# Kernel tuning notes

Measured on AMD Instinct MI355X. Metric: run time of the kernel, lower is better.

## Reference

```python
import jax, jax.numpy as jnp
import numpy as np
import math

N_NODES, N_EDGES, NNZ, D, L = 100000, 20000, 500000, 128, 4
ALPHA, LAMDA = 0.1, 0.5


def setup_inputs() -> dict:
    key = jax.random.key(0)
    ks = jax.random.split(key, 16)
    x = jax.random.normal(ks[0], (N_NODES, D), jnp.float32)
    e = jax.random.normal(ks[1], (N_EDGES, D), jnp.float32)
    nodes = jax.random.randint(ks[2], (NNZ,), 0, N_NODES)
    edges = jnp.sort(jax.random.randint(ks[3], (NNZ,), 0, N_EDGES)).at[-1].set(N_EDGES - 1)
    hyperedge_index = jnp.stack([nodes, edges]).astype(jnp.int32)
    dist_v2e = jax.random.randint(ks[4], (NNZ,), 0, 64).astype(jnp.float32)
    deg_v2e = jax.random.randint(ks[5], (NNZ,), 0, 64).astype(jnp.float32)
    dist_e2v = jax.random.randint(ks[6], (NNZ,), 0, 64).astype(jnp.float32)
    deg_e2v = jax.random.randint(ks[7], (NNZ,), 0, 64).astype(jnp.float32)
    s = 0.05
    W0 = jax.random.normal(ks[8], (D, D), jnp.float32) * s
    b0 = jnp.zeros((D,), jnp.float32)
    Wn = jax.random.normal(ks[9], (L, D, D), jnp.float32) * s
    We = jax.random.normal(ks[10], (L, D, D), jnp.float32) * s
    attn_w = jax.random.normal(ks[11], (L, 2 * D), jnp.float32) * s
    attn_b = jnp.zeros((L,), jnp.float32)
    wd_w = jax.random.normal(ks[12], (L,), jnp.float32) * s
    wd_b = jnp.zeros((L,), jnp.float32)
    wg_w = jax.random.normal(ks[13], (L,), jnp.float32) * s
    wg_b = jnp.zeros((L,), jnp.float32)
    return dict(x=x, e=e, hyperedge_index=hyperedge_index, dist_v2e=dist_v2e,
                deg_v2e=deg_v2e, dist_e2v=dist_e2v, deg_e2v=deg_e2v,
                W0=W0, b0=b0, Wn=Wn, We=We, attn_w=attn_w, attn_b=attn_b,
                wd_w=wd_w, wd_b=wd_b, wg_w=wg_w, wg_b=wg_b)


def _seg_softmax(s, idx, num):
    # numerically-stable scatter_softmax over segments idx
    m = jax.ops.segment_max(s, idx, num_segments=num)
    ex = jnp.exp(s - m[idx])
    den = jax.ops.segment_sum(ex, idx, num_segments=num)
    return ex / den[idx]


def _forward(x, e, hei, dv2e, gv2e, de2v, ge2v, W0, b0, Wn, We, aw, ab, wdw, wdb, wgw, wgb):
    nodes, edges = hei[0], hei[1]
    N, E = x.shape[0], e.shape[0]
    ones = jnp.ones(nodes.shape[0], x.dtype)
    dV = jax.ops.segment_sum(ones, nodes, num_segments=N)
    cnt = jax.ops.segment_sum(ones, edges, num_segments=E)
    dE = jax.ops.segment_sum(dV[nodes], edges, num_segments=E) / jnp.maximum(cnt, 1.0)
    degV = jnp.where(dV > 0, dV ** -0.5, 1.0)[:, None]   # [N,1]
    degE = jnp.where(dE > 0, dE ** -0.5, 1.0)[:, None]   # [E,1]

    x = jax.nn.relu(x @ W0 + b0)
    x0, e0 = x, e
    d = x.shape[1]
    for i in range(L):
        beta = math.log(LAMDA / (i + 1) + 1.0)
        # v2e attention: concat [x[nodes], e[edges]] -> softmax over edge segments
        sx1 = x @ aw[i, :d]; se1 = e @ aw[i, d:]
        s_v2e = sx1[nodes] + se1[edges] + ab[i] + dv2e * wdw[i] + wdb[i] + gv2e * wgw[i] + wgb[i]
        a_v2e = _seg_softmax(s_v2e, edges, E)[:, None]
        # e2v attention (flipped): concat [e[edges], x[nodes]] -> softmax over node segments
        se2 = e @ aw[i, :d]; sx2 = x @ aw[i, d:]
        s_e2v = se2[edges] + sx2[nodes] + ab[i] + de2v * wdw[i] + wdb[i] + ge2v * wgw[i] + wgb[i]
        a_e2v = _seg_softmax(s_e2v, nodes, N)[:, None]

        Xe1 = jax.ops.segment_sum(x[nodes] * a_v2e, edges, num_segments=E) * degE
        Xv1 = jax.ops.segment_sum(Xe1[edges] * a_e2v, nodes, num_segments=N) * degV
        Xv2 = jax.ops.segment_sum(e[edges] * a_e2v, nodes, num_segments=N) * degV
        Xe2 = jax.ops.segment_sum(Xv2[nodes] * a_v2e, edges, num_segments=E) * degE
        xm = (Xv1 + Xv2) * 0.5
        em = (Xe1 + Xe2) * 0.5
        xi = (1 - ALPHA) * xm + ALPHA * x0
        x = (1 - beta) * xi + beta * (xi @ Wn[i])
        ei = (1 - ALPHA) * em + ALPHA * e0
        e = (1 - beta) * ei + beta * (ei @ We[i])
        if i < L - 1:
            x = jax.nn.relu(x)
            e = jax.nn.relu(e)
    return x, e


def reference(x, e, hyperedge_index, dist_v2e, deg_v2e, dist_e2v, deg_e2v,
              W0, b0, Wn, We, attn_w, attn_b, wd_w, wd_b, wg_w, wg_b):
    return _forward(x, e, hyperedge_index, dist_v2e, deg_v2e, dist_e2v, deg_e2v,
                    W0, b0, Wn, We, attn_w, attn_b, wd_w, wd_b, wg_w, wg_b)
```

## Files before the change

### kernel.cpp

```cpp
#include <hip/hip_runtime.h>
#include <hip/hip_fp16.h>
#include <math.h>

#define DD 128
#define SCAN_BLOCKS 256
#define SMAX_CAP 128

typedef _Float16 f16x8 __attribute__((ext_vector_type(8)));
typedef float f32x4 __attribute__((ext_vector_type(4)));

__device__ inline float wave_sum(float v){
#pragma unroll
  for (int m = 32; m >= 1; m >>= 1) v += __shfl_xor(v, m, 64);
  return v;
}
__device__ inline int wave_sum_i(int v){
#pragma unroll
  for (int m = 32; m >= 1; m >>= 1) v += __shfl_xor(v, m, 64);
  return v;
}


__global__ void k_edge_offsets(const int* __restrict__ edges, int nnz, int E,
                               int* __restrict__ eo){
  int e = blockIdx.x * blockDim.x + threadIdx.x;
  if (e > E) return;
  int lo = 0, hi = nnz;
  while (lo < hi){ int mid = (lo + hi) >> 1; if (edges[mid] < e) lo = mid + 1; else hi = mid; }
  eo[e] = lo;
}

__global__ void k_hist(const int* __restrict__ nodes, int nnz, int* __restrict__ dV){
  int k = blockIdx.x * blockDim.x + threadIdx.x;
  if (k < nnz) atomicAdd(&dV[nodes[k]], 1);
}

__global__ __launch_bounds__(256) void k_scan_partial(const int* __restrict__ dV, int N,
                                                      int* __restrict__ part){
  int b = blockIdx.x, t = threadIdx.x;
  int chunk = (N + SCAN_BLOCKS - 1) / SCAN_BLOCKS;
  int s0 = b * chunk, s1 = min(s0 + chunk, N);
  int sum = 0;
  for (int n = s0 + t; n < s1; n += 256) sum += dV[n];
  sum = wave_sum_i(sum);
  __shared__ int wred[4];
  int lane = t & 63, wid = t >> 6;
  if (lane == 0) wred[wid] = sum;
  __syncthreads();
  if (t == 0) part[b] = wred[0] + wred[1] + wred[2] + wred[3];
}

__global__ __launch_bounds__(SCAN_BLOCKS) void k_scan_blocksums(int* __restrict__ part){
  __shared__ int sh[SCAN_BLOCKS];
  int t = threadIdx.x;
  int v = part[t];
  sh[t] = v; __syncthreads();
  for (int off = 1; off < SCAN_BLOCKS; off <<= 1){
    int add = (t >= off) ? sh[t - off] : 0;
    __syncthreads();
    sh[t] += add;
    __syncthreads();
  }
  part[t] = sh[t] - v;
}

__global__ __launch_bounds__(256) void k_scan_apply(const int* __restrict__ dV, int N, int nnz,
    const int* __restrict__ partScan, int* __restrict__ no, int* __restrict__ nfill,
    float* __restrict__ degV){
  int b = blockIdx.x, t = threadIdx.x;
  int chunk = (N + SCAN_BLOCKS - 1) / SCAN_BLOCKS;
  int s0 = b * chunk, s1 = min(s0 + chunk, N);
  int lane = t & 63, wid = t >> 6;
  __shared__ int wtot[4];
  __shared__ int s_run;
  if (t == 0) s_run = partScan[b];
  __syncthreads();
  for (int base = s0; base < s1; base += 256){
    int n = base + t;
    int d = (n < s1) ? dV[n] : 0;
    int v = d;
#pragma unroll
    for (int off = 1; off < 64; off <<= 1){
      int o = __shfl_up(v, off, 64);
      if (lane >= off) v += o;
    }
    if (lane == 63) wtot[wid] = v;
    __syncthreads();
    int run0 = s_run;
    int woff = 0;
    for (int w = 0; w < wid; w++) woff += wtot[w];
    if (n < s1){
      int excl = run0 + woff + v - d;
      no[n] = excl; nfill[n] = excl;
      degV[n] = d > 0 ? 1.0f / sqrtf((float)d) : 1.0f;
    }
    int btot = wtot[0] + wtot[1] + wtot[2] + wtot[3];
    __syncthreads();
    if (t == 0) s_run = run0 + btot;
    __syncthreads();
  }
  if (b == 0 && t == 0) no[N] = nnz;
}

__global__ void k_permpack(const int* __restrict__ nodes, const int* __restrict__ edges,
                           const float* __restrict__ dist, const float* __restrict__ deg,
                           int nnz, int* __restrict__ nfill, float2* __restrict__ pack){
  int k = blockIdx.x * blockDim.x + threadIdx.x;
  if (k < nnz){
    int pos = atomicAdd(&nfill[nodes[k]], 1);
    pack[pos] = make_float2(__int_as_float(edges[k]), dist[k] + 64.f * deg[k]);
  }
}

__global__ void k_edge_deg(const int* __restrict__ nodes, const int* __restrict__ eo, int E,
                           const int* __restrict__ dV, float* __restrict__ degE){
  int e = blockIdx.x * blockDim.x + threadIdx.x;
  if (e >= E) return;
  int b = eo[e], en = eo[e + 1];
  float s = 0.f;
  for (int k = b; k < en; k++) s += (float)dV[nodes[k]];
  float cnt = (float)(en - b);
  float dE = s / fmaxf(cnt, 1.0f);
  degE[e] = dE > 0.f ? 1.0f / sqrtf(dE) : 1.0f;
}

__global__ __launch_bounds__(256) void k_einit(const float2* __restrict__ e_in2,
    const float* __restrict__ aw1, const float* __restrict__ aw2,
    int E, __half2* __restrict__ ET, __half2* __restrict__ e0h,
    float* __restrict__ se1, float* __restrict__ se2){
  int wave = threadIdx.x >> 6, lane = threadIdx.x & 63;
  int e = blockIdx.x * 4 + wave;
  if (e >= E) return;
  float2 v = e_in2[(size_t)e * 64 + lane];
  __half2 h = __floats2half2_rn(v.x, v.y);
  ET[(size_t)e * 128 + 2 * lane + 1] = h;
  e0h[(size_t)e * 64 + lane] = h;
  float2 a2v = ((const float2*)aw2)[lane];
  float2 a1v = ((const float2*)aw1)[lane];
  float s1 = v.x * a2v.x + v.y * a2v.y;
  float s2 = v.x * a1v.x + v.y * a1v.y;
  s1 = wave_sum(s1); s2 = wave_sum(s2);
  if (lane == 0){ se1[e] = s1; se2[e] = s2; }
}

__global__ void k_wcast(const float* __restrict__ W0, const float* __restrict__ Wn,
                        const float* __restrict__ We, _Float16* __restrict__ Wt){
  int idx = blockIdx.x * 256 + threadIdx.x;
  if (idx >= 9 * 16384) return;
  int m = idx >> 14, r = idx & 16383;
  int n = r >> 7, k = r & 127;
  float v;
  if (m == 0){
    v = W0[k * 128 + n];
  } else {
    int i = (m <= 4) ? m - 1 : m - 5;
    const float* src = (m <= 4) ? Wn + (size_t)i * 16384 : We + (size_t)i * 16384;
    float beta = logf(0.5f / (float)(i + 1) + 1.0f);
    v = beta * src[k * 128 + n] + ((n == k) ? (1.0f - beta) : 0.f);
  }
  Wt[(size_t)m * 16384 + n * 128 + k] = (_Float16)v;
}


__device__ inline void acc8h(const float4 q, float w, float* a){
  float2 h0 = __half22float2(*(const __half2*)&q.x);
  float2 h1 = __half22float2(*(const __half2*)&q.y);
  float2 h2v = __half22float2(*(const __half2*)&q.z);
  float2 h3 = __half22float2(*(const __half2*)&q.w);
  a[0] += w * h0.x; a[1] += w * h0.y; a[2] += w * h1.x; a[3] += w * h1.y;
  a[4] += w * h2v.x; a[5] += w * h2v.y; a[6] += w * h3.x; a[7] += w * h3.y;
}

__global__ __launch_bounds__(256) void k_sma1(
    const int* __restrict__ nodes, const int* __restrict__ eo,
    const float* __restrict__ sx1, const float* __restrict__ se1,
    const float* __restrict__ dist, const float* __restrict__ deg,
    const float* __restrict__ ab, const float* __restrict__ wdw, const float* __restrict__ wdb,
    const float* __restrict__ wgw, const float* __restrict__ wgb, int li,
    const float* __restrict__ degE, const float4* __restrict__ xh4,
    int E, float* __restrict__ a_v2e, float* __restrict__ esc, __half2* __restrict__ ET){
  __shared__ float lw[8][SMAX_CAP];
  int l32 = threadIdx.x & 31;
  int grp = threadIdx.x >> 5;
  int e = blockIdx.x * 8 + grp;
  if (e >= E) return;
  int b = eo[e], en = eo[e + 1];
  int l16 = l32 & 15, hf = l32 >> 4;
  if (b >= en){
    if (l32 == 0) esc[e] = 0.f;
    if (hf == 0){
      __half2 z = __floats2half2_rn(0.f, 0.f);
      size_t o = (size_t)e * 128 + 8 * l16;
      ET[o] = z; ET[o + 2] = z; ET[o + 4] = z; ET[o + 6] = z;
    }
    return;
  }
  float base = se1[e] + ab[li] + wdb[li] + wgb[li];
  float wd = wdw[li], wg = wgw[li];
  float m = -INFINITY;
  float sreg[4];
#pragma unroll
  for (int c = 0; c < 4; c++){
    int k = b + l32 + 32 * c;
    if (k < en){
      float s = sx1[nodes[k]] + base + dist[k] * wd + deg[k] * wg;
      sreg[c] = s; m = fmaxf(m, s);
    }
  }
  for (int k = b + l32 + SMAX_CAP; k < en; k += 32){
    float s = sx1[nodes[k]] + base + dist[k] * wd + deg[k] * wg;
    m = fmaxf(m, s);
  }
#pragma unroll
  for (int mm = 16; mm >= 1; mm >>= 1) m = fmaxf(m, __shfl_xor(m, mm, 32));
  float sum = 0.f;
#pragma unroll
  for (int c = 0; c < 4; c++){
    int k = b + l32 + 32 * c;
    if (k < en){
      float ex = __expf(sreg[c] - m);
      a_v2e[k] = ex; lw[grp][l32 + 32 * c] = ex; sum += ex;
    }
  }
  for (int k = b + l32 + SMAX_CAP; k < en; k += 32){
    float s = sx1[nodes[k]] + base + dist[k] * wd + deg[k] * wg;
    float ex = __expf(s - m);
    a_v2e[k] = ex; sum += ex;
  }
#pragma unroll
  for (int mm = 16; mm >= 1; mm >>= 1) sum += __shfl_xor(sum, mm, 32);
  float sc = degE[e] / sum;
  if (l32 == 0) esc[e] = sc;
  float a[8] = {0.f, 0.f, 0.f, 0.f, 0.f, 0.f, 0.f, 0.f};
  int k = b + hf;
  for (; k + 2 < en; k += 4){
    int n0 = nodes[k], n1 = nodes[k + 2];
    float w0 = (k - b < SMAX_CAP) ? lw[grp][k - b] : a_v2e[k];
    float w1 = (k + 2 - b < SMAX_CAP) ? lw[grp][k + 2 - b] : a_v2e[k + 2];
    float4 v0 = xh4[(size_t)n0 * 16 + l16];
    float4 v1 = xh4[(size_t)n1 * 16 + l16];
    acc8h(v0, w0, a); acc8h(v1, w1, a);
  }
  for (; k < en; k += 2){
    int n = nodes[k];
    float w = (k - b < SMAX_CAP) ? lw[grp][k - b] : a_v2e[k];
    float4 v = xh4[(size_t)n * 16 + l16];
    acc8h(v, w, a);
  }
#pragma unroll
  for (int j = 0; j < 8; j++) a[j] += __shfl_xor(a[j], 16, 32);
  if (hf == 0){
    size_t o = (size_t)e * 128 + 8 * l16;
    ET[o]     = __floats2half2_rn(a[0] * sc, a[1] * sc);
    ET[o + 2] = __floats2half2_rn(a[2] * sc, a[3] * sc);
    ET[o + 4] = __floats2half2_rn(a[4] * sc, a[5] * sc);
    ET[o + 6] = __floats2half2_rn(a[6] * sc, a[7] * sc);
  }
}

__device__ inline void acc8(const float4 q, float w, float* a1, float* a2){
  float2 x0 = __half22float2(*(const __half2*)&q.x);
  float2 e0 = __half22float2(*(const __half2*)&q.y);
  float2 x1 = __half22float2(*(const __half2*)&q.z);
  float2 e1 = __half22float2(*(const __half2*)&q.w);
  a1[0] += w * x0.x; a1[1] += w * x0.y; a1[2] += w * x1.x; a1[3] += w * x1.y;
  a2[0] += w * e0.x; a2[1] += w * e0.y; a2[2] += w * e1.x; a2[3] += w * e1.y;
}

__global__ __launch_bounds__(256) void k_agg2f(
    const float2* __restrict__ pack, const int* __restrict__ no,
    const float* __restrict__ se2, const float* __restrict__ sx2,
    const float* __restrict__ ab, const float* __restrict__ wdw, const float* __restrict__ wdb,
    const float* __restrict__ wgw, const float* __restrict__ wgb, int li,
    const float4* __restrict__ ETq,
    const float* __restrict__ degV, const __half2* __restrict__ x0h,
    int N, __half2* __restrict__ Xv2h, __half2* __restrict__ xiH){
  int l32 = threadIdx.x & 31;
  int grp = threadIdx.x >> 5;
  int n = blockIdx.x * 8 + grp;
  if (n >= N) return;
  int b = no[n], en = no[n + 1];
  float base = sx2[n] + ab[li] + wdb[li] + wgb[li];
  float wd = wdw[li], wg = wgw[li];
  float2 x0v2 = *(const float2*)&x0h[(size_t)n * 64 + 2 * l32];
  float l_run = 0.f;
  float a1[4] = {0.f, 0.f, 0.f, 0.f}, a2[4] = {0.f, 0.f, 0.f, 0.f};
  if (en - b <= 32){
    int cs = en - b;
    float s = -INFINITY; int e_l = 0;
    if (l32 < cs){
      float2 pk = pack[b + l32];
      e_l = __float_as_int(pk.x);
      int vi = (int)pk.y;
      s = se2[e_l] + base + (float)(vi & 63) * wd + (float)(vi >> 6) * wg;
    }
    float m_c = s;
#pragma unroll
    for (int mm = 16; mm >= 1; mm >>= 1) m_c = fmaxf(m_c, __shfl_xor(m_c, mm, 32));
    float p = (l32 < cs) ? __expf(s - m_c) : 0.f;
    l_run = p;
#pragma unroll
    for (int mm = 16; mm >= 1; mm >>= 1) l_run += __shfl_xor(l_run, mm, 32);
    int jj = 0;
    for (; jj + 7 < cs; jj += 8){
      float w[8]; int ei[8]; float4 q[8];
#pragma unroll
      for (int u = 0; u < 8; u++){
        w[u] = __shfl(p, jj + u, 32);
        ei[u] = __shfl(e_l, jj + u, 32);
      }
#pragma unroll
      for (int u = 0; u < 8; u++) q[u] = ETq[(size_t)ei[u] * 32 + l32];
#pragma unroll
      for (int u = 0; u < 8; u++) acc8(q[u], w[u], a1, a2);
    }
    for (; jj + 3 < cs; jj += 4){
      float w[4]; int ei[4]; float4 q[4];
#pragma unroll
      for (int u = 0; u < 4; u++){
        w[u] = __shfl(p, jj + u, 32);
        ei[u] = __shfl(e_l, jj + u, 32);
      }
#pragma unroll
      for (int u = 0; u < 4; u++) q[u] = ETq[(size_t)ei[u] * 32 + l32];
#pragma unroll
      for (int u = 0; u < 4; u++) acc8(q[u], w[u], a1, a2);
    }
    for (; jj < cs; jj++){
      float w = __shfl(p, jj, 32);
      int ei_ = __shfl(e_l, jj, 32);
      float4 q = ETq[(size_t)ei_ * 32 + l32];
      acc8(q, w, a1, a2);
    }
  } else {
    float m_run = -INFINITY;
    for (int cb = b; cb < en; cb += 32){
      int cs = min(32, en - cb);
      float s = -INFINITY; int e_l = 0;
      if (l32 < cs){
        float2 pk = pack[cb + l32];
        e_l = __float_as_int(pk.x);
        int vi = (int)pk.y;
        s = se2[e_l] + base + (float)(vi & 63) * wd + (float)(vi >> 6) * wg;
      }
      float m_c = s;
#pragma unroll
      for (int mm = 16; mm >= 1; mm >>= 1) m_c = fmaxf(m_c, __shfl_xor(m_c, mm, 32));
      float p = (l32 < cs) ? __expf(s - m_c) : 0.f;
      float l_c = p;
#pragma unroll
      for (int mm = 16; mm >= 1; mm >>= 1) l_c += __shfl_xor(l_c, mm, 32);
      float m_new = fmaxf(m_run, m_c);
      float f_old = __expf(m_run - m_new);
      float f_c = __expf(m_c - m_new);
#pragma unroll
      for (int r = 0; r < 4; r++){ a1[r] *= f_old; a2[r] *= f_old; }
      l_run = l_run * f_old + l_c * f_c;
      m_run = m_new;
      int jj = 0;
      for (; jj + 3 < cs; jj += 4){
        float w0 = __shfl(p, jj, 32) * f_c;
        float w1 = __shfl(p, jj + 1, 32) * f_c;
        float w2 = __shfl(p, jj + 2, 32) * f_c;
        float w3 = __shfl(p, jj + 3, 32) * f_c;
        int e0i = __shfl(e_l, jj, 32);
        int e1i = __shfl(e_l, jj + 1, 32);
        int e2i = __shfl(e_l, jj + 2, 32);
        int e3i = __shfl(e_l, jj + 3, 32);
        float4 q0 = ETq[(size_t)e0i * 32 + l32];
        float4 q1 = ETq[(size_t)e1i * 32 + l32];
        float4 q2 = ETq[(size_t)e2i * 32 + l32];
        float4 q3 = ETq[(size_t)e3i * 32 + l32];
        acc8(q0, w0, a1, a2);
        acc8(q1, w1, a1, a2);
        acc8(q2, w2, a1, a2);
        acc8(q3, w3, a1, a2);
      }
      for (; jj < cs; jj++){
        float w = __shfl(p, jj, 32) * f_c;
        int ei_ = __shfl(e_l, jj, 32);
        float4 q = ETq[(size_t)ei_ * 32 + l32];
        acc8(q, w, a1, a2);
      }
    }
  }
  float inv = l_run > 0.f ? 1.0f / l_run : 0.f;
  float dv = degV[n] * inv;
  float2 st;
  *(__half2*)&st.x = __floats2half2_rn(a2[0] * dv, a2[1] * dv);
  *(__half2*)&st.y = __floats2half2_rn(a2[2] * dv, a2[3] * dv);
  *(float2*)&Xv2h[(size_t)n * 64 + 2 * l32] = st;
  float2 h0 = __half22float2(*(const __half2*)&x0v2.x);
  float2 h1 = __half22float2(*(const __half2*)&x0v2.y);
  float2 xo;
  *(__half2*)&xo.x = __floats2half2_rn(0.45f * dv * (a1[0] + a2[0]) + 0.1f * h0.x,
                                       0.45f * dv * (a1[1] + a2[1]) + 0.1f * h0.y);
  *(__half2*)&xo.y = __floats2half2_rn(0.45f * dv * (a1[2] + a2[2]) + 0.1f * h1.x,
                                       0.45f * dv * (a1[3] + a2[3]) + 0.1f * h1.y);
  *(float2*)&xiH[(size_t)n * 64 + 2 * l32] = xo;
}

__device__ __forceinline__ void gemm_body(
    const _Float16* __restrict__ Ah, const _Float16* __restrict__ Wt,
    float* __restrict__ outf, _Float16* __restrict__ outh, int et,
    const float* __restrict__ awA, const float* __restrict__ awB,
    float* __restrict__ sA, float* __restrict__ sB,
    int nrows, int do_relu, int row0){
  int lane = threadIdx.x & 63;
  int lm = lane & 15;
  int lk8 = (lane >> 4) * 8;
  int arow = row0 + lm; if (arow >= nrows) arow = nrows - 1;
  f16x8 afrag[4];
#pragma unroll
  for (int ks = 0; ks < 4; ks++)
    afrag[ks] = *(const f16x8*)(Ah + (size_t)arow * 128 + ks * 32 + lk8);
  int rbase = (lane >> 4) * 4;
  float da[4] = {0.f, 0.f, 0.f, 0.f}, db[4] = {0.f, 0.f, 0.f, 0.f};
  for (int t = 0; t < 8; t++){
    f32x4 acc = {0.f, 0.f, 0.f, 0.f};
#pragma unroll
    for (int ks = 0; ks < 4; ks++){
      f16x8 bf = *(const f16x8*)(Wt + (size_t)(t * 16 + lm) * 128 + ks * 32 + lk8);
      acc = __builtin_amdgcn_mfma_f32_16x16x32_f16(afrag[ks], bf, acc, 0, 0, 0);
    }
    int col = t * 16 + lm;
    float wa = 0.f, wb = 0.f;
    if (awA){ wa = awA[col]; wb = awB[col]; }
#pragma unroll
    for (int r = 0; r < 4; r++){
      int gr = row0 + rbase + r;
      if (gr >= nrows) continue;
      float v = acc[r];
      if (do_relu) v = fmaxf(v, 0.f);
      if (outf) outf[(size_t)gr * 128 + col] = v;
      if (outh){
        if (et) outh[(size_t)gr * 256 + (col >> 1) * 4 + 2 + (col & 1)] = (_Float16)v;
        else    outh[(size_t)gr * 128 + col] = (_Float16)v;
      }
      da[r] += v * wa; db[r] += v * wb;
    }
  }
  if (awA){
#pragma unroll
    for (int r = 0; r < 4; r++){
      float a = da[r], bb = db[r];
#pragma unroll
      for (int m = 8; m >= 1; m >>= 1){
        a += __shfl_xor(a, m, 64);
        bb += __shfl_xor(bb, m, 64);
      }
      int gr = row0 + rbase + r;
      if (lm == 0 && gr < nrows){ sA[gr] = a; sB[gr] = bb; }
    }
  }
}

__global__ __launch_bounds__(256) void k_a3gx(
    const int* __restrict__ nodes, const int* __restrict__ eo,
    const float4* __restrict__ Xv2h4, const float* __restrict__ a_v2e,
    const float* __restrict__ esc,
    const float4* __restrict__ ETq, const float4* __restrict__ e0h4,
    int E, __half2* __restrict__ eiH, int nbA,
    const _Float16* __restrict__ Ah, const _Float16* __restrict__ Wt,
    float* __restrict__ outf, _Float16* __restrict__ outh,
    const float* __restrict__ awA, const float* __restrict__ awB,
    float* __restrict__ sA, float* __restrict__ sB, int N, int do_relu){
  if ((int)blockIdx.x >= nbA){
    int row0 = (blockIdx.x - nbA) * 64 + (threadIdx.x >> 6) * 16;
    if (row0 >= N) return;
    gemm_body(Ah, Wt, outf, outh, 0, awA, awB, sA, sB, N, do_relu, row0);
    return;
  }
  int l32 = threadIdx.x & 31;
  int grp = threadIdx.x >> 5;
  int e = blockIdx.x * 8 + grp;
  if (e >= E) return;
  int b = eo[e], en = eo[e + 1];
  int l16 = l32 & 15, hf = l32 >> 4;
  float a[8] = {0.f, 0.f, 0.f, 0.f, 0.f, 0.f, 0.f, 0.f};
  int k = b + hf;
  for (; k + 2 < en; k += 4){
    int n0 = nodes[k], n1 = nodes[k + 2];
    float w0 = a_v2e[k], w1 = a_v2e[k + 2];
    float4 v0 = Xv2h4[(size_t)n0 * 16 + l16];
    float4 v1 = Xv2h4[(size_t)n1 * 16 + l16];
    acc8h(v0, w0, a); acc8h(v1, w1, a);
  }
  for (; k < en; k += 2){
    int n = nodes[k];
    float w = a_v2e[k];
    float4 v = Xv2h4[(size_t)n * 16 + l16];
    acc8h(v, w, a);
  }
#pragma unroll
  for (int j = 0; j < 8; j++) a[j] += __shfl_xor(a[j], 16, 32);
  if (hf == 0){
    float dE = esc[e];
    float4 q0 = ETq[(size_t)e * 32 + 2 * l16];
    float4 q1 = ETq[(size_t)e * 32 + 2 * l16 + 1];
    float2 x01 = __half22float2(*(const __half2*)&q0.x);
    float2 x23 = __half22float2(*(const __half2*)&q0.z);
    float2 x45 = __half22float2(*(const __half2*)&q1.x);
    float2 x67 = __half22float2(*(const __half2*)&q1.z);
    float4 ev = e0h4[(size_t)e * 16 + l16];
    float2 g0 = __half22float2(*(const __half2*)&ev.x);
    float2 g1 = __half22float2(*(const __half2*)&ev.y);
    float2 g2 = __half22float2(*(const __half2*)&ev.z);
    float2 g3 = __half22float2(*(const __half2*)&ev.w);
    float4 o;
    *(__half2*)&o.x = __floats2half2_rn(0.45f * (x01.x + a[0] * dE) + 0.1f * g0.x,
                                        0.45f * (x01.y + a[1] * dE) + 0.1f * g0.y);
    *(__half2*)&o.y = __floats2half2_rn(0.45f * (x23.x + a[2] * dE) + 0.1f * g1.x,
                                        0.45f * (x23.y + a[3] * dE) + 0.1f * g1.y);
    *(__half2*)&o.z = __floats2half2_rn(0.45f * (x45.x + a[4] * dE) + 0.1f * g2.x,
                                        0.45f * (x45.y + a[5] * dE) + 0.1f * g2.y);
    *(__half2*)&o.w = __floats2half2_rn(0.45f * (x67.x + a[6] * dE) + 0.1f * g3.x,
                                        0.45f * (x67.y + a[7] * dE) + 0.1f * g3.y);
    *(float4*)&eiH[(size_t)e * 64 + 4 * l16] = o;
  }
}

__global__ __launch_bounds__(256) void k_gemme(
    const _Float16* __restrict__ Ah, const _Float16* __restrict__ Wt,
    float* __restrict__ outf, _Float16* __restrict__ outh,
    const float* __restrict__ awA, const float* __restrict__ awB,
    float* __restrict__ sA, float* __restrict__ sB, int nrows, int do_relu){
  int row0 = blockIdx.x * 64 + (threadIdx.x >> 6) * 16;
  if (row0 >= nrows) return;
  gemm_body(Ah, Wt, outf, outh, 1, awA, awB, sA, sB, nrows, do_relu, row0);
}

__global__ __launch_bounds__(256) void k_gemm0(
    const float* __restrict__ Af, const _Float16* __restrict__ Wt,
    const float* __restrict__ bias,
    _Float16* __restrict__ outh, _Float16* __restrict__ outh2,
    const float* __restrict__ awA, const float* __restrict__ awB,
    float* __restrict__ sA, float* __restrict__ sB, int nrows){
  int wave = threadIdx.x >> 6, lane = threadIdx.x & 63;
  int row0 = blockIdx.x * 64 + wave * 16;
  if (row0 >= nrows) return;
  int lm = lane & 15;
  int lk8 = (lane >> 4) * 8;
  int arow = row0 + lm; if (arow >= nrows) arow = nrows - 1;
  const float* ap = Af + (size_t)arow * 128;
  f16x8 afrag[4];
#pragma unroll
  for (int ks = 0; ks < 4; ks++){
    float4 v0 = *(const float4*)(ap + ks * 32 + lk8);
    float4 v1 = *(const float4*)(ap + ks * 32 + lk8 + 4);
    f16x8 a;
    a[0] = (_Float16)v0.x; a[1] = (_Float16)v0.y; a[2] = (_Float16)v0.z; a[3] = (_Float16)v0.w;
    a[4] = (_Float16)v1.x; a[5] = (_Float16)v1.y; a[6] = (_Float16)v1.z; a[7] = (_Float16)v1.w;
    afrag[ks] = a;
  }
  int rbase = (lane >> 4) * 4;
  float da[4] = {0.f, 0.f, 0.f, 0.f}, db[4] = {0.f, 0.f, 0.f, 0.f};
  for (int t = 0; t < 8; t++){
    f32x4 acc = {0.f, 0.f, 0.f, 0.f};
#pragma unroll
    for (int ks = 0; ks < 4; ks++){
      f16x8 bf = *(const f16x8*)(Wt + (size_t)(t * 16 + lm) * 128 + ks * 32 + lk8);
      acc = __builtin_amdgcn_mfma_f32_16x16x32_f16(afrag[ks], bf, acc, 0, 0, 0);
    }
    int col = t * 16 + lm;
    float wa = awA[col], wb = awB[col];
    float bi = bias[col];
#pragma unroll
    for (int r = 0; r < 4; r++){
      int gr = row0 + rbase + r;
      if (gr >= nrows) continue;
      float v = fmaxf(acc[r] + bi, 0.f);
      outh[(size_t)gr * 128 + col] = (_Float16)v;
      outh2[(size_t)gr * 128 + col] = (_Float16)v;
      da[r] += v * wa; db[r] += v * wb;
    }
  }
#pragma unroll
  for (int r = 0; r < 4; r++){
    float a = da[r], bb = db[r];
#pragma unroll
    for (int m = 8; m >= 1; m >>= 1){
      a += __shfl_xor(a, m, 64);
      bb += __shfl_xor(bb, m, 64);
    }
    int gr = row0 + rbase + r;
    if (lm == 0 && gr < nrows){ sA[gr] = a; sB[gr] = bb; }
  }
}


extern "C" void kernel_launch(void* const* d_in, const int* in_sizes, int n_in,
                              void* d_out, int out_size, void* d_ws, size_t ws_size,
                              hipStream_t stream) {
  const float* x_in     = (const float*)d_in[0];
  const float* e_in     = (const float*)d_in[1];
  const int*   hei      = (const int*)d_in[2];
  const float* dist_v2e = (const float*)d_in[3];
  const float* deg_v2e  = (const float*)d_in[4];
  const float* dist_e2v = (const float*)d_in[5];
  const float* deg_e2v  = (const float*)d_in[6];
  const float* W0       = (const float*)d_in[7];
  const float* b0       = (const float*)d_in[8];
  const float* Wn       = (const float*)d_in[9];
  const float* We       = (const float*)d_in[10];
  const float* attn_w   = (const float*)d_in[11];
  const float* attn_b   = (const float*)d_in[12];
  const float* wd_w     = (const float*)d_in[13];
  const float* wd_b     = (const float*)d_in[14];
  const float* wg_w     = (const float*)d_in[15];
  const float* wg_b     = (const float*)d_in[16];

  const int N   = in_sizes[0] / DD;
  const int E   = in_sizes[1] / DD;
  const int NNZ = in_sizes[2] / 2;
  const int* nodesArr = hei;
  const int* edgesArr = hei + NNZ;

  float* out_x = (float*)d_out;
  float* out_e = (float*)d_out + (size_t)N * DD;

  __half2* xh   = (__half2*)((char*)out_x + (size_t)N * DD * 2);
  __half2* ET   = (__half2*)out_e;
  const float4* ETq = (const float4*)out_e;

  char* wsp = (char*)d_ws;
  auto alloc = [&](size_t bytes) -> void* {
    void* p = (void*)wsp;
    wsp += (bytes + 255) / 256 * 256;
    return p;
  };
  _Float16* x0h  = (_Float16*)alloc((size_t)N * DD * 2);
  _Float16* Xv2h = (_Float16*)alloc((size_t)N * DD * 2);
  _Float16* xiH  = (_Float16*)alloc((size_t)N * DD * 2);
  _Float16* eiH  = (_Float16*)alloc((size_t)E * DD * 2);
  _Float16* e0h  = (_Float16*)alloc((size_t)E * DD * 2);
  _Float16* Wt   = (_Float16*)alloc((size_t)9 * 16384 * 2);
  float* sx1   = (float*)alloc((size_t)N * 4);
  float* sx2   = (float*)alloc((size_t)N * 4);
  float* se1   = (float*)alloc((size_t)E * 4);
  float* se2   = (float*)alloc((size_t)E * 4);
  float* a_v2e = (float*)alloc((size_t)NNZ * 4);
  float* degV  = (float*)alloc((size_t)N * 4);
  float* degE  = (float*)alloc((size_t)E * 4);
  float* esc   = (float*)alloc((size_t)E * 4);
  float2* pack = (float2*)alloc((size_t)NNZ * 8);
  int* dV_i  = (int*)alloc((size_t)N * 4);
  int* no_   = (int*)alloc((size_t)(N + 1) * 4);
  int* nfill = (int*)alloc((size_t)N * 4);
  int* eo    = (int*)alloc((size_t)(E + 1) * 4);
  int* part  = (int*)alloc((size_t)SCAN_BLOCKS * 4);

  hipMemsetAsync(dV_i, 0, (size_t)N * 4, stream);
  k_edge_offsets<<<(E + 1 + 255) / 256, 256, 0, stream>>>(edgesArr, NNZ, E, eo);
  k_hist<<<(NNZ + 255) / 256, 256, 0, stream>>>(nodesArr, NNZ, dV_i);
  k_scan_partial<<<SCAN_BLOCKS, 256, 0, stream>>>(dV_i, N, part);
  k_scan_blocksums<<<1, SCAN_BLOCKS, 0, stream>>>(part);
  k_scan_apply<<<SCAN_BLOCKS, 256, 0, stream>>>(dV_i, N, NNZ, part, no_, nfill, degV);
  k_permpack<<<(NNZ + 255) / 256, 256, 0, stream>>>(nodesArr, edgesArr, dist_e2v, deg_e2v,
                                                    NNZ, nfill, pack);
  k_edge_deg<<<(E + 255) / 256, 256, 0, stream>>>(nodesArr, eo, E, dV_i, degE);
  k_wcast<<<(9 * 16384 + 255) / 256, 256, 0, stream>>>(W0, Wn, We, Wt);

  const float* aw1_0 = attn_w;
  const float* aw2_0 = attn_w + 128;

  k_einit<<<(E + 3) / 4, 256, 0, stream>>>((const float2*)e_in, aw1_0, aw2_0,
                                            E, ET, (__half2*)e0h, se1, se2);

  k_gemm0<<<(N + 63) / 64, 256, 0, stream>>>(x_in, Wt, b0,
      (_Float16*)xh, x0h, aw1_0, aw2_0, sx1, sx2, N);

  const int nbA = (E + 7) / 8, nbG = (N + 63) / 64;
  for (int i = 0; i < 4; i++){
    const float* aw1n = (i < 3) ? attn_w + (size_t)(i + 1) * 256        : nullptr;
    const float* aw2n = (i < 3) ? attn_w + (size_t)(i + 1) * 256 + 128  : nullptr;

    k_sma1<<<(E + 7) / 8, 256, 0, stream>>>(nodesArr, eo, sx1, se1,
        dist_v2e, deg_v2e, attn_b, wd_w, wd_b, wg_w, wg_b, i, degE,
        (const float4*)xh, E, a_v2e, esc, ET);

    k_agg2f<<<(N + 7) / 8, 256, 0, stream>>>(pack, no_, se2, sx2,
        attn_b, wd_w, wd_b, wg_w, wg_b, i,
        ETq, degV, (const __half2*)x0h, N, (__half2*)Xv2h, (__half2*)xiH);

    k_a3gx<<<nbA + nbG, 256, 0, stream>>>(
        nodesArr, eo, (const float4*)Xv2h, a_v2e, esc, ETq, (const float4*)e0h,
        E, (__half2*)eiH, nbA,
        xiH, Wt + (size_t)(1 + i) * 16384,
        (i == 3) ? out_x : nullptr, (i < 3) ? (_Float16*)xh : nullptr,
        aw1n, aw2n, sx1, sx2, N, i < 3 ? 1 : 0);

    k_gemme<<<(E + 63) / 64, 256, 0, stream>>>(eiH, Wt + (size_t)(5 + i) * 16384,
        (i == 3) ? out_e : nullptr, (i < 3) ? (_Float16*)ET : nullptr,
        aw2n, aw1n, se1, se2, E, i < 3 ? 1 : 0);
  }
}
```

Measured before the change: 864.8 us.

## Regroup layer kernels: fuse node and edge GEMMs, stage GEMM outputs via LDS

Restructures each layer's launch schedule. The edge aggregation (agg3) now runs as its own kernel, and the node-side and edge-side GEMMs are merged into one launch (k_gemm2). GEMM outputs are staged through shared memory and written as coalesced 16-byte rows, replacing scattered 2-byte stores. The interleaved edge-feature buffer ET is no longer written with strided halves by the GEMM; the edge GEMM writes a dense buffer (ehL), and k_sma1 interleaves it with its own result using vector stores. This costs an extra E×128 half buffer, one more read in sma1, and a __syncthreads in the GEMMs.

After: 825.7 us. 1.05x faster.

```diff
diff --git a/kernel.cpp b/kernel.cpp
--- a/kernel.cpp
+++ b/kernel.cpp
@@ -126,15 +126,13 @@
 
 __global__ __launch_bounds__(256) void k_einit(const float2* __restrict__ e_in2,
     const float* __restrict__ aw1, const float* __restrict__ aw2,
-    int E, __half2* __restrict__ ET, __half2* __restrict__ e0h,
+    int E, __half2* __restrict__ e0h,
     float* __restrict__ se1, float* __restrict__ se2){
   int wave = threadIdx.x >> 6, lane = threadIdx.x & 63;
   int e = blockIdx.x * 4 + wave;
   if (e >= E) return;
   float2 v = e_in2[(size_t)e * 64 + lane];
-  __half2 h = __floats2half2_rn(v.x, v.y);
-  ET[(size_t)e * 128 + 2 * lane + 1] = h;
-  e0h[(size_t)e * 64 + lane] = h;
+  e0h[(size_t)e * 64 + lane] = __floats2half2_rn(v.x, v.y);
   float2 a2v = ((const float2*)aw2)[lane];
   float2 a1v = ((const float2*)aw1)[lane];
   float s1 = v.x * a2v.x + v.y * a2v.y;
@@ -178,7 +176,8 @@
     const float* __restrict__ ab, const float* __restrict__ wdw, const float* __restrict__ wdb,
     const float* __restrict__ wgw, const float* __restrict__ wgb, int li,
     const float* __restrict__ degE, const float4* __restrict__ xh4,
-    int E, float* __restrict__ a_v2e, float* __restrict__ esc, __half2* __restrict__ ET){
+    const _Float16* __restrict__ ehL,
+    int E, float* __restrict__ a_v2e, float* __restrict__ esc, _Float16* __restrict__ ETraw){
   __shared__ float lw[8][SMAX_CAP];
   int l32 = threadIdx.x & 31;
   int grp = threadIdx.x >> 5;
@@ -189,9 +188,17 @@
   if (b >= en){
     if (l32 == 0) esc[e] = 0.f;
     if (hf == 0){
-      __half2 z = __floats2half2_rn(0.f, 0.f);
-      size_t o = (size_t)e * 128 + 8 * l16;
-      ET[o] = z; ET[o + 2] = z; ET[o + 4] = z; ET[o + 6] = z;
+      f16x8 ehv = *(const f16x8*)(ehL + (size_t)e * 128 + 8 * l16);
+      f16x8 o0, o1;
+#pragma unroll
+      for (int q = 0; q < 2; q++){
+        o0[4 * q] = (_Float16)0.f; o0[4 * q + 1] = (_Float16)0.f;
+        o0[4 * q + 2] = ehv[2 * q]; o0[4 * q + 3] = ehv[2 * q + 1];
+        o1[4 * q] = (_Float16)0.f; o1[4 * q + 1] = (_Float16)0.f;
+        o1[4 * q + 2] = ehv[2 * q + 4]; o1[4 * q + 3] = ehv[2 * q + 5];
+      }
+      _Float16* dst = ETraw + (size_t)e * 256 + 16 * l16;
+      *(f16x8*)dst = o0; *(f16x8*)(dst + 8) = o1;
     }
     return;
   }
@@ -250,11 +257,19 @@
 #pragma unroll
   for (int j = 0; j < 8; j++) a[j] += __shfl_xor(a[j], 16, 32);
   if (hf == 0){
-    size_t o = (size_t)e * 128 + 8 * l16;
-    ET[o]     = __floats2half2_rn(a[0] * sc, a[1] * sc);
-    ET[o + 2] = __floats2half2_rn(a[2] * sc, a[3] * sc);
-    ET[o + 4] = __floats2half2_rn(a[4] * sc, a[5] * sc);
-    ET[o + 6] = __floats2half2_rn(a[6] * sc, a[7] * sc);
+    f16x8 ehv = *(const f16x8*)(ehL + (size_t)e * 128 + 8 * l16);
+    f16x8 o0, o1;
+#pragma unroll
+    for (int q = 0; q < 2; q++){
+      __half2 xa = __floats2half2_rn(a[2 * q] * sc, a[2 * q + 1] * sc);
+      o0[4 * q] = ((_Float16*)&xa)[0]; o0[4 * q + 1] = ((_Float16*)&xa)[1];
+      o0[4 * q + 2] = ehv[2 * q]; o0[4 * q + 3] = ehv[2 * q + 1];
+      __half2 xb = __floats2half2_rn(a[2 * q + 4] * sc, a[2 * q + 5] * sc);
+      o1[4 * q] = ((_Float16*)&xb)[0]; o1[4 * q + 1] = ((_Float16*)&xb)[1];
+      o1[4 * q + 2] = ehv[2 * q + 4]; o1[4 * q + 3] = ehv[2 * q + 5];
+    }
+    _Float16* dst = ETraw + (size_t)e * 256 + 16 * l16;
+    *(f16x8*)dst = o0; *(f16x8*)(dst + 8) = o1;
   }
 }
 
@@ -400,77 +415,10 @@
   *(float2*)&xiH[(size_t)n * 64 + 2 * l32] = xo;
 }
 
-__device__ __forceinline__ void gemm_body(
-    const _Float16* __restrict__ Ah, const _Float16* __restrict__ Wt,
-    float* __restrict__ outf, _Float16* __restrict__ outh, int et,
-    const float* __restrict__ awA, const float* __restrict__ awB,
-    float* __restrict__ sA, float* __restrict__ sB,
-    int nrows, int do_relu, int row0){
-  int lane = threadIdx.x & 63;
-  int lm = lane & 15;
-  int lk8 = (lane >> 4) * 8;
-  int arow = row0 + lm; if (arow >= nrows) arow = nrows - 1;
-  f16x8 afrag[4];
-#pragma unroll
-  for (int ks = 0; ks < 4; ks++)
-    afrag[ks] = *(const f16x8*)(Ah + (size_t)arow * 128 + ks * 32 + lk8);
-  int rbase = (lane >> 4) * 4;
-  float da[4] = {0.f, 0.f, 0.f, 0.f}, db[4] = {0.f, 0.f, 0.f, 0.f};
-  for (int t = 0; t < 8; t++){
-    f32x4 acc = {0.f, 0.f, 0.f, 0.f};
-#pragma unroll
-    for (int ks = 0; ks < 4; ks++){
-      f16x8 bf = *(const f16x8*)(Wt + (size_t)(t * 16 + lm) * 128 + ks * 32 + lk8);
-      acc = __builtin_amdgcn_mfma_f32_16x16x32_f16(afrag[ks], bf, acc, 0, 0, 0);
-    }
-    int col = t * 16 + lm;
-    float wa = 0.f, wb = 0.f;
-    if (awA){ wa = awA[col]; wb = awB[col]; }
-#pragma unroll
-    for (int r = 0; r < 4; r++){
-      int gr = row0 + rbase + r;
-      if (gr >= nrows) continue;
-      float v = acc[r];
-      if (do_relu) v = fmaxf(v, 0.f);
-      if (outf) outf[(size_t)gr * 128 + col] = v;
-      if (outh){
-        if (et) outh[(size_t)gr * 256 + (col >> 1) * 4 + 2 + (col & 1)] = (_Float16)v;
-        else    outh[(size_t)gr * 128 + col] = (_Float16)v;
-      }
-      da[r] += v * wa; db[r] += v * wb;
-    }
-  }
-  if (awA){
-#pragma unroll
-    for (int r = 0; r < 4; r++){
-      float a = da[r], bb = db[r];
-#pragma unroll
-      for (int m = 8; m >= 1; m >>= 1){
-        a += __shfl_xor(a, m, 64);
-        bb += __shfl_xor(bb, m, 64);
-      }
-      int gr = row0 + rbase + r;
-      if (lm == 0 && gr < nrows){ sA[gr] = a; sB[gr] = bb; }
-    }
-  }
-}
-
-__global__ __launch_bounds__(256) void k_a3gx(
-    const int* __restrict__ nodes, const int* __restrict__ eo,
-    const float4* __restrict__ Xv2h4, const float* __restrict__ a_v2e,
-    const float* __restrict__ esc,
+__global__ __launch_bounds__(256) void k_agg3(const int* __restrict__ nodes, const int* __restrict__ eo,
+    const float4* __restrict__ Xv2h4, const float* __restrict__ a_v2e, const float* __restrict__ esc,
     const float4* __restrict__ ETq, const float4* __restrict__ e0h4,
-    int E, __half2* __restrict__ eiH, int nbA,
-    const _Float16* __restrict__ Ah, const _Float16* __restrict__ Wt,
-    float* __restrict__ outf, _Float16* __restrict__ outh,
-    const float* __restrict__ awA, const float* __restrict__ awB,
-    float* __restrict__ sA, float* __restrict__ sB, int N, int do_relu){
-  if ((int)blockIdx.x >= nbA){
-    int row0 = (blockIdx.x - nbA) * 64 + (threadIdx.x >> 6) * 16;
-    if (row0 >= N) return;
-    gemm_body(Ah, Wt, outf, outh, 0, awA, awB, sA, sB, N, do_relu, row0);
-    return;
-  }
+    int E, __half2* __restrict__ eiH){
   int l32 = threadIdx.x & 31;
   int grp = threadIdx.x >> 5;
   int e = blockIdx.x * 8 + grp;
@@ -520,14 +468,87 @@
   }
 }
 
-__global__ __launch_bounds__(256) void k_gemme(
+__device__ __forceinline__ void gemm_body(
     const _Float16* __restrict__ Ah, const _Float16* __restrict__ Wt,
     float* __restrict__ outf, _Float16* __restrict__ outh,
     const float* __restrict__ awA, const float* __restrict__ awB,
-    float* __restrict__ sA, float* __restrict__ sB, int nrows, int do_relu){
-  int row0 = blockIdx.x * 64 + (threadIdx.x >> 6) * 16;
-  if (row0 >= nrows) return;
-  gemm_body(Ah, Wt, outf, outh, 1, awA, awB, sA, sB, nrows, do_relu, row0);
+    float* __restrict__ sA, float* __restrict__ sB,
+    int nrows, int do_relu, int blockRow0, _Float16 (*sh)[136]){
+  int lane = threadIdx.x & 63, wave = threadIdx.x >> 6;
+  int row0 = blockRow0 + wave * 16;
+  int lm = lane & 15;
+  int lk8 = (lane >> 4) * 8;
+  int rbase = (lane >> 4) * 4;
+  if (row0 < nrows){
+    int arow = row0 + lm; if (arow >= nrows) arow = nrows - 1;
+    f16x8 afrag[4];
+#pragma unroll
+    for (int ks = 0; ks < 4; ks++)
+      afrag[ks] = *(const f16x8*)(Ah + (size_t)arow * 128 + ks * 32 + lk8);
+    float da[4] = {0.f, 0.f, 0.f, 0.f}, db[4] = {0.f, 0.f, 0.f, 0.f};
+    for (int t = 0; t < 8; t++){
+      f32x4 acc = {0.f, 0.f, 0.f, 0.f};
+#pragma unroll
+      for (int ks = 0; ks < 4; ks++){
+        f16x8 bf = *(const f16x8*)(Wt + (size_t)(t * 16 + lm) * 128 + ks * 32 + lk8);
+        acc = __builtin_amdgcn_mfma_f32_16x16x32_f16(afrag[ks], bf, acc, 0, 0, 0);
+      }
+      int col = t * 16 + lm;
+      float wa = 0.f, wb = 0.f;
+      if (awA){ wa = awA[col]; wb = awB[col]; }
+#pragma unroll
+      for (int r = 0; r < 4; r++){
+        int gr = row0 + rbase + r;
+        float v = acc[r];
+        if (do_relu) v = fmaxf(v, 0.f);
+        if (outf && gr < nrows) outf[(size_t)gr * 128 + col] = v;
+        if (outh) sh[wave * 16 + rbase + r][col] = (_Float16)v;
+        if (gr < nrows){ da[r] += v * wa; db[r] += v * wb; }
+      }
+    }
+    if (awA){
+#pragma unroll
+      for (int r = 0; r < 4; r++){
+        float a = da[r], bb = db[r];
+#pragma unroll
+        for (int m = 8; m >= 1; m >>= 1){
+          a += __shfl_xor(a, m, 64);
+          bb += __shfl_xor(bb, m, 64);
+        }
+        int gr = row0 + rbase + r;
+        if (lm == 0 && gr < nrows){ sA[gr] = a; sB[gr] = bb; }
+      }
+    }
+  }
+  if (outh){
+    __syncthreads();
+    for (int i = threadIdx.x; i < 64 * 16; i += 256){
+      int rr = i >> 4, cc = (i & 15) * 8;
+      int gr = blockRow0 + rr;
+      if (gr < nrows)
+        *(f16x8*)(outh + (size_t)gr * 128 + cc) = *(const f16x8*)&sh[rr][cc];
+    }
+  }
+}
+
+__global__ __launch_bounds__(256) void k_gemm2(
+    const _Float16* __restrict__ Ax, const _Float16* __restrict__ Wx,
+    const _Float16* __restrict__ Ae, const _Float16* __restrict__ Wte,
+    float* __restrict__ outfx, _Float16* __restrict__ outhx,
+    float* __restrict__ outfe, _Float16* __restrict__ outhe,
+    const float* __restrict__ awAx, const float* __restrict__ awBx,
+    float* __restrict__ sAx, float* __restrict__ sBx,
+    const float* __restrict__ awAe, const float* __restrict__ awBe,
+    float* __restrict__ sAe, float* __restrict__ sBe,
+    int nrx, int nre, int nbx, int do_relu){
+  __shared__ _Float16 sh[64][136];
+  if ((int)blockIdx.x < nbx){
+    gemm_body(Ax, Wx, outfx, outhx, awAx, awBx, sAx, sBx, nrx, do_relu,
+              blockIdx.x * 64, sh);
+  } else {
+    gemm_body(Ae, Wte, outfe, outhe, awAe, awBe, sAe, sBe, nre, do_relu,
+              (blockIdx.x - nbx) * 64, sh);
+  }
 }
 
 __global__ __launch_bounds__(256) void k_gemm0(
@@ -536,55 +557,66 @@
     _Float16* __restrict__ outh, _Float16* __restrict__ outh2,
     const float* __restrict__ awA, const float* __restrict__ awB,
     float* __restrict__ sA, float* __restrict__ sB, int nrows){
+  __shared__ _Float16 sh[64][136];
   int wave = threadIdx.x >> 6, lane = threadIdx.x & 63;
-  int row0 = blockIdx.x * 64 + wave * 16;
-  if (row0 >= nrows) return;
+  int blockRow0 = blockIdx.x * 64;
+  int row0 = blockRow0 + wave * 16;
   int lm = lane & 15;
   int lk8 = (lane >> 4) * 8;
-  int arow = row0 + lm; if (arow >= nrows) arow = nrows - 1;
-  const float* ap = Af + (size_t)arow * 128;
-  f16x8 afrag[4];
-#pragma unroll
-  for (int ks = 0; ks < 4; ks++){
-    float4 v0 = *(const float4*)(ap + ks * 32 + lk8);
-    float4 v1 = *(const float4*)(ap + ks * 32 + lk8 + 4);
-    f16x8 a;
-    a[0] = (_Float16)v0.x; a[1] = (_Float16)v0.y; a[2] = (_Float16)v0.z; a[3] = (_Float16)v0.w;
-    a[4] = (_Float16)v1.x; a[5] = (_Float16)v1.y; a[6] = (_Float16)v1.z; a[7] = (_Float16)v1.w;
-    afrag[ks] = a;
-  }
   int rbase = (lane >> 4) * 4;
-  float da[4] = {0.f, 0.f, 0.f, 0.f}, db[4] = {0.f, 0.f, 0.f, 0.f};
-  for (int t = 0; t < 8; t++){
-    f32x4 acc = {0.f, 0.f, 0.f, 0.f};
+  if (row0 < nrows){
+    int arow = row0 + lm; if (arow >= nrows) arow = nrows - 1;
+    const float* ap = Af + (size_t)arow * 128;
+    f16x8 afrag[4];
 #pragma unroll
     for (int ks = 0; ks < 4; ks++){
-      f16x8 bf = *(const f16x8*)(Wt + (size_t)(t * 16 + lm) * 128 + ks * 32 + lk8);
-      acc = __builtin_amdgcn_mfma_f32_16x16x32_f16(afrag[ks], bf, acc, 0, 0, 0);
-    }
-    int col = t * 16 + lm;
-    float wa = awA[col], wb = awB[col];
-    float bi = bias[col];
+      float4 v0 = *(const float4*)(ap + ks * 32 + lk8);
+      float4 v1 = *(const float4*)(ap + ks * 32 + lk8 + 4);
+      f16x8 a;
+      a[0] = (_Float16)v0.x; a[1] = (_Float16)v0.y; a[2] = (_Float16)v0.z; a[3] = (_Float16)v0.w;
+      a[4] = (_Float16)v1.x; a[5] = (_Float16)v1.y; a[6] = (_Float16)v1.z; a[7] = (_Float16)v1.w;
+      afrag[ks] = a;
+    }
+    float da[4] = {0.f, 0.f, 0.f, 0.f}, db[4] = {0.f, 0.f, 0.f, 0.f};
+    for (int t = 0; t < 8; t++){
+      f32x4 acc = {0.f, 0.f, 0.f, 0.f};
+#pragma unroll
+      for (int ks = 0; ks < 4; ks++){
+        f16x8 bf = *(const f16x8*)(Wt + (size_t)(t * 16 + lm) * 128 + ks * 32 + lk8);
+        acc = __builtin_amdgcn_mfma_f32_16x16x32_f16(afrag[ks], bf, acc, 0, 0, 0);
+      }
+      int col = t * 16 + lm;
+      float wa = awA[col], wb = awB[col];
+      float bi = bias[col];
+#pragma unroll
+      for (int r = 0; r < 4; r++){
+        int gr = row0 + rbase + r;
+        float v = fmaxf(acc[r] + bi, 0.f);
+        sh[wave * 16 + rbase + r][col] = (_Float16)v;
+        if (gr < nrows){ da[r] += v * wa; db[r] += v * wb; }
+      }
+    }
 #pragma unroll
     for (int r = 0; r < 4; r++){
+      float a = da[r], bb = db[r];
+#pragma unroll
+      for (int m = 8; m >= 1; m >>= 1){
+        a += __shfl_xor(a, m, 64);
+        bb += __shfl_xor(bb, m, 64);
+      }
       int gr = row0 + rbase + r;
-      if (gr >= nrows) continue;
-      float v = fmaxf(acc[r] + bi, 0.f);
-      outh[(size_t)gr * 128 + col] = (_Float16)v;
-      outh2[(size_t)gr * 128 + col] = (_Float16)v;
-      da[r] += v * wa; db[r] += v * wb;
-    }
-  }
-#pragma unroll
-  for (int r = 0; r < 4; r++){
-    float a = da[r], bb = db[r];
-#pragma unroll
-    for (int m = 8; m >= 1; m >>= 1){
-      a += __shfl_xor(a, m, 64);
-      bb += __shfl_xor(bb, m, 64);
-    }
-    int gr = row0 + rbase + r;
-    if (lm == 0 && gr < nrows){ sA[gr] = a; sB[gr] = bb; }
+      if (lm == 0 && gr < nrows){ sA[gr] = a; sB[gr] = bb; }
+    }
+  }
+  __syncthreads();
+  for (int i = threadIdx.x; i < 64 * 16; i += 256){
+    int rr = i >> 4, cc = (i & 15) * 8;
+    int gr = blockRow0 + rr;
+    if (gr < nrows){
+      f16x8 v = *(const f16x8*)&sh[rr][cc];
+      *(f16x8*)(outh + (size_t)gr * 128 + cc) = v;
+      *(f16x8*)(outh2 + (size_t)gr * 128 + cc) = v;
+    }
   }
 }
 
@@ -620,7 +652,7 @@
   float* out_e = (float*)d_out + (size_t)N * DD;
 
   __half2* xh   = (__half2*)((char*)out_x + (size_t)N * DD * 2);
-  __half2* ET   = (__half2*)out_e;
+  _Float16* ETraw = (_Float16*)out_e;
   const float4* ETq = (const float4*)out_e;
 
   char* wsp = (char*)d_ws;
@@ -634,6 +666,7 @@
   _Float16* xiH  = (_Float16*)alloc((size_t)N * DD * 2);
   _Float16* eiH  = (_Float16*)alloc((size_t)E * DD * 2);
   _Float16* e0h  = (_Float16*)alloc((size_t)E * DD * 2);
+  _Float16* ehL  = (_Float16*)alloc((size_t)E * DD * 2);
   _Float16* Wt   = (_Float16*)alloc((size_t)9 * 16384 * 2);
   float* sx1   = (float*)alloc((size_t)N * 4);
   float* sx2   = (float*)alloc((size_t)N * 4);
@@ -665,33 +698,35 @@
   const float* aw2_0 = attn_w + 128;
 
   k_einit<<<(E + 3) / 4, 256, 0, stream>>>((const float2*)e_in, aw1_0, aw2_0,
-                                            E, ET, (__half2*)e0h, se1, se2);
+                                            E, (__half2*)e0h, se1, se2);
 
   k_gemm0<<<(N + 63) / 64, 256, 0, stream>>>(x_in, Wt, b0,
       (_Float16*)xh, x0h, aw1_0, aw2_0, sx1, sx2, N);
 
-  const int nbA = (E + 7) / 8, nbG = (N + 63) / 64;
+  const int nbx = (N + 63) / 64, nbe = (E + 63) / 64;
   for (int i = 0; i < 4; i++){
     const float* aw1n = (i < 3) ? attn_w + (size_t)(i + 1) * 256        : nullptr;
     const float* aw2n = (i < 3) ? attn_w + (size_t)(i + 1) * 256 + 128  : nullptr;
+    const _Float16* ehCur = (i == 0) ? e0h : ehL;
 
     k_sma1<<<(E + 7) / 8, 256, 0, stream>>>(nodesArr, eo, sx1, se1,
         dist_v2e, deg_v2e, attn_b, wd_w, wd_b, wg_w, wg_b, i, degE,
-        (const float4*)xh, E, a_v2e, esc, ET);
+        (const float4*)xh, ehCur, E, a_v2e, esc, ETraw);
 
     k_agg2f<<<(N + 7) / 8, 256, 0, stream>>>(pack, no_, se2, sx2,
         attn_b, wd_w, wd_b, wg_w, wg_b, i,
         ETq, degV, (const __half2*)x0h, N, (__half2*)Xv2h, (__half2*)xiH);
 
-    k_a3gx<<<nbA + nbG, 256, 0, stream>>>(
-        nodesArr, eo, (const float4*)Xv2h, a_v2e, esc, ETq, (const float4*)e0h,
-        E, (__half2*)eiH, nbA,
+    k_agg3<<<(E + 7) / 8, 256, 0, stream>>>(nodesArr, eo, (const float4*)Xv2h,
+        a_v2e, esc, ETq, (const float4*)e0h, E, (__half2*)eiH);
+
+    k_gemm2<<<nbx + nbe, 256, 0, stream>>>(
         xiH, Wt + (size_t)(1 + i) * 16384,
+        eiH, Wt + (size_t)(5 + i) * 16384,
         (i == 3) ? out_x : nullptr, (i < 3) ? (_Float16*)xh : nullptr,
-        aw1n, aw2n, sx1, sx2, N, i < 3 ? 1 : 0);
-
-    k_gemme<<<(E + 63) / 64, 256, 0, stream>>>(eiH, Wt + (size_t)(5 + i) * 16384,
-        (i == 3) ? out_e : nullptr, (i < 3) ? (_Float16*)ET : nullptr,
-        aw2n, aw1n, se1, se2, E, i < 3 ? 1 : 0);
-  }
-}
+        (i == 3) ? out_e : nullptr, (i < 3) ? ehL : nullptr,
+        aw1n, aw2n, sx1, sx2,
+        aw2n, aw1n, se1, se2,
+        N, E, nbx, i < 3 ? 1 : 0);
+  }
+}
```
